# Optimization experiments

Hardware: AMD Instinct MI355X
Metric: run time of the kernel (lower is better)

## Reference

```python
import jax, jax.numpy as jnp
import numpy as np

NOISE = 0.02
P_CONST = 1.0
NUM_LAYERS = 7


def setup_inputs() -> dict:
    key = jax.random.key(0)
    k1, k2, k3, k4 = jax.random.split(key, 4)
    B, Nt, K, L = 2048, 64, 40, NUM_LAYERS
    sqrtP = np.sqrt(P_CONST)
    return {
        'H_real': jax.random.normal(k1, (B, Nt, K), dtype=jnp.float32),
        'H_imag': jax.random.normal(k2, (B, Nt, K), dtype=jnp.float32),
        'eta': jnp.ones((L,), dtype=jnp.float32) * (0.1 / sqrtP),
        'U': jax.random.normal(k3, (L, Nt, Nt), dtype=jnp.float32) * (0.01 / sqrtP),
        'b': jax.random.normal(k4, (L, Nt, K), dtype=jnp.float32) * (0.01 / sqrtP),
    }


def _rate_total(Wr, Wi, Hc):
    # sum over batch of (sum_k log2(1+sinr_k) - power_penalty)
    W = Wr + 1j * Wi                                   # [B,Nt,K] complex
    HW = jnp.einsum('bnk,bnl->bkl', jnp.conj(Hc), W)   # [B,K,K]
    pw = jnp.abs(HW) ** 2                              # |h_k^H w_l|^2
    desired = jnp.diagonal(pw, axis1=1, axis2=2)       # [B,K]
    interference = pw.sum(axis=2) - desired
    sinr = desired / (interference + NOISE)
    rates = jnp.log2(1.0 + sinr).sum()
    power = jnp.sum(Wr * Wr + Wi * Wi, axis=(1, 2))    # ||W||_F^2 per batch
    penalty = jnp.mean((power - P_CONST) ** 2) * 0.01
    B = Wr.shape[0]
    return rates - B * penalty


def reference(H_real, H_imag, eta, U, b):
    Hc = H_real + 1j * H_imag
    B, Nt, K = H_real.shape
    Wr = jnp.zeros((B, Nt, K), dtype=jnp.float32)
    Wi = jnp.zeros((B, Nt, K), dtype=jnp.float32)
    grad_fn = jax.grad(_rate_total, argnums=(0, 1))
    for t in range(NUM_LAYERS):
        g_r, g_i = grad_fn(Wr, Wi, Hc)                 # torch grad: dL/dx + i dL/dy
        Ug_r = jnp.einsum('nm,bmk->bnk', U[t], g_r)
        Ug_i = jnp.einsum('nm,bmk->bnk', U[t], g_i)
        step_r = Ug_r - Ug_i
        step_i = Ug_i + Ug_r
        Wr = Wr - eta[t] * step_r + b[t]
        Wi = Wi - eta[t] * step_i
    # final power normalization
    norm = jnp.sqrt(jnp.sum(Wr * Wr + Wi * Wi, axis=(1, 2), keepdims=True))
    scale = jnp.sqrt(P_CONST) / (norm + 1e-6)
    Wr = Wr * scale
    Wi = Wi * scale
    return Wr + 1j * Wi
```

## Files before the change

kernel.cpp:

```cpp
#include <hip/hip_runtime.h>
#include <math.h>

typedef _Float16 h16;
typedef __attribute__((ext_vector_type(2))) _Float16 h16x2;
typedef __attribute__((ext_vector_type(4))) _Float16 h16x4;
typedef __attribute__((ext_vector_type(8))) _Float16 h16x8;
typedef __attribute__((ext_vector_type(4))) float f32x4;

#define NBATCH 2048
#define NT 64
#define KK 40
#define NL 7
#define SIGMA 0.02f
#define INVLN2 1.4426950408889634f

#define WT   0
#define HCK  (48*128)
#define HNC  (HCK + 48*128)
#define B2T  (HNC + 64*128)
#define GRE  B2T
#define GIM  (B2T + 48*64)
#define UOF  (B2T + 48*128)
#define LDSH (UOF + 64*64)

#define SWZ(row, c)  ((c) ^ (((row)&7)<<3))
#define SWZW(row, c) ((c) ^ (((row)&15)<<3))
#define MFMA16(a,b,c) __builtin_amdgcn_mfma_f32_16x16x32_f16((a),(b),(c),0,0,0)

static __device__ __forceinline__ float DOT2(h16x2 a, h16x2 b, float c) {
#if __has_builtin(__builtin_amdgcn_fdot2)
    return __builtin_amdgcn_fdot2(a, b, c, false);
#else
    return fmaf((float)a.x, (float)b.x, fmaf((float)a.y, (float)b.y, c));
#endif
}
static __device__ __forceinline__ h16x2 PK(float x, float y) {
    h16x2 r; r.x = (h16)x; r.y = (h16)y; return r;
}
static __device__ __forceinline__ h16x8 conjA(h16x8 v) {
    union { h16x8 h; unsigned u[4]; } x; x.h = v;
    #pragma unroll
    for (int i=0;i<4;++i){ unsigned t=x.u[i]; t=(t>>16)|(t<<16); x.u[i]=t^0x80000000u; }
    return x.h;
}
static __device__ __forceinline__ h16x8 imB(h16x8 v) {
    union { h16x8 h; unsigned u[4]; } x; x.h = v;
    #pragma unroll
    for (int i=0;i<4;++i){ unsigned t=x.u[i]; t=(t>>16)|(t<<16); x.u[i]=t^0x00008000u; }
    return x.h;
}

__global__ __launch_bounds__(256, 2) void gpnet_kernel(
    const float* __restrict__ gHr, const float* __restrict__ gHi,
    const float* __restrict__ gEta, const float* __restrict__ gU,
    const float* __restrict__ gB, float* __restrict__ gOut, int outFloats)
{
    __shared__ __align__(16) h16 sh[LDSH];
    __shared__ float sRed[4];

    const int tid = threadIdx.x;
    const int wv  = tid >> 6;
    const int ln  = tid & 63;
    const int col = ln & 15;
    const int g   = ln >> 4;

    const int bb = blockIdx.x;
    const float* hr = gHr + (size_t)bb * NT * KK;
    const float* hi = gHi + (size_t)bb * NT * KK;

    for (int i = tid; i < 512; i += 256) {
        *(h16x2*)(sh + WT  + 40*128 + 2*i) = PK(0.f, 0.f);
        *(h16x2*)(sh + HCK + 40*128 + 2*i) = PK(0.f, 0.f);
    }
    for (int i = tid; i < 512; i += 256) {
        int n = i >> 3, c = 80 + 2*(i & 7);
        *(h16x2*)(sh + HNC + n*128 + SWZ(n, c)) = PK(0.f, 0.f);
    }
    for (int i = tid; i < NT*KK; i += 256) {
        int n = i / KK, k = i % KK;
        float xr = hr[i], xi = hi[i];
        h16x2 p = PK(xr, xi);
        *(h16x2*)(sh + HCK + k*128 + SWZW(k, 2*n)) = p;
        *(h16x2*)(sh + HNC + n*128 + SWZ(n, 2*k)) = p;
        *(h16x2*)(sh + WT  + k*128 + SWZW(k, 2*n)) = PK(gB[i], 0.f);
    }
    float Wr[3][4], Wi[3][4];
    float ps = 0.f;
    #pragma unroll
    for (int ct = 0; ct < 3; ++ct)
        #pragma unroll
        for (int r = 0; r < 4; ++r) {
            int n = 16*wv + 4*g + r, l = col + 16*ct;
            float b0 = (l < KK) ? gB[n*KK + l] : 0.f;
            Wr[ct][r] = b0; Wi[ct][r] = 0.f;
            ps += b0 * b0;
        }
    #pragma unroll
    for (int off = 32; off; off >>= 1) ps += __shfl_down(ps, off, 64);
    if (ln == 0) sRed[wv] = ps;
    __syncthreads();

    for (int t = 1; t < NL; ++t) {
        const float pw   = sRed[0] + sRed[1] + sRed[2] + sRed[3];
        const float cpen = 0.04f * (pw - 1.0f);
        const float etat = gEta[t];

        float2 ureg[8];
        {
            const float2* u2 = (const float2*)(gU + (size_t)t * NT * NT);
            #pragma unroll
            for (int j = 0; j < 8; ++j) ureg[j] = u2[tid + j*256];
        }
        float breg[3][4];
        #pragma unroll
        for (int ct = 0; ct < 3; ++ct)
            #pragma unroll
            for (int r = 0; r < 4; ++r) {
                int n = 16*wv + 4*g + r, l = col + 16*ct;
                breg[ct][r] = (l < KK) ? gB[(size_t)t*NT*KK + n*KK + l] : 0.f;
            }

        if (wv < 3) {
            f32x4 aRe[3], aIm[3];
            #pragma unroll
            for (int rt = 0; rt < 3; ++rt) { aRe[rt] = (f32x4){0.f,0.f,0.f,0.f}; aIm[rt] = (f32x4){0.f,0.f,0.f,0.f}; }
            const int kcol = col + 16*wv;
            #pragma unroll
            for (int q = 0; q < 4; ++q) {
                h16x8 bf = *(const h16x8*)(sh + HCK + kcol*128 + SWZW(kcol, g*8 + 32*q));
                #pragma unroll
                for (int rt = 0; rt < 3; ++rt) {
                    int lrow = col + 16*rt;
                    h16x8 af = *(const h16x8*)(sh + WT + lrow*128 + SWZW(lrow, g*8 + 32*q));
                    aRe[rt] = MFMA16(af, bf, aRe[rt]);
                    aIm[rt] = MFMA16(conjA(af), bf, aIm[rt]);
                }
            }
            #pragma unroll
            for (int rt = 0; rt < 3; ++rt)
                #pragma unroll
                for (int r = 0; r < 4; ++r) {
                    int l = 16*rt + 4*g + r;
                    *(h16x2*)(sh + B2T + l*128 + SWZ(l, 2*kcol)) =
                        PK(aRe[rt][r], aIm[rt][r]);
                }
        }
        __syncthreads();

        if (tid < 160) {
            const int k = tid >> 2, q = tid & 3;
            h16x2 va[10];
            #pragma unroll
            for (int ii = 0; ii < 10; ++ii)
                va[ii] = *(const h16x2*)(sh + B2T + (q*10+ii)*128 + SWZ(q*10+ii, 2*k));
            float rs = 0.f, dd = 0.f;
            #pragma unroll
            for (int ii = 0; ii < 10; ++ii) rs = DOT2(va[ii], va[ii], rs);
            const int dk = k - q*10;
            if (dk >= 0 && dk < 10) dd = DOT2(va[dk], va[dk], 0.f);
            rs += __shfl_xor(rs, 1, 64); rs += __shfl_xor(rs, 2, 64);
            dd += __shfl_xor(dd, 1, 64); dd += __shfl_xor(dd, 2, 64);
            float T  = rs + SIGMA, Is = rs - dd + SIGMA;
            float cA_ = 2.f * INVLN2 / T;
            float cC_ = -2.f * INVLN2 * dd / (Is * T);
            #pragma unroll
            for (int ii = 0; ii < 10; ++ii) {
                int l = q*10 + ii;
                float c = (l == k) ? cA_ : cC_;
                *(h16x2*)(sh + B2T + l*128 + SWZ(l, 2*k)) =
                    PK((float)va[ii].x * c, -(float)va[ii].y * c);
            }
        }
        __syncthreads();

        f32x4 gRe[3], gIm[3];
        #pragma unroll
        for (int ct = 0; ct < 3; ++ct) { gRe[ct] = (f32x4){0.f,0.f,0.f,0.f}; gIm[ct] = (f32x4){0.f,0.f,0.f,0.f}; }
        {
            const int nrow = col + 16*wv;
            #pragma unroll
            for (int q = 0; q < 3; ++q) {
                h16x8 af = *(const h16x8*)(sh + HNC + nrow*128 + SWZ(nrow, g*8 + 32*q));
                #pragma unroll
                for (int ct = 0; ct < 3; ++ct) {
                    int lr = col + 16*ct;
                    h16x8 bf = *(const h16x8*)(sh + B2T + lr*128 + SWZ(lr, g*8 + 32*q));
                    gRe[ct] = MFMA16(af, bf, gRe[ct]);
                    gIm[ct] = MFMA16(af, imB(bf), gIm[ct]);
                }
            }
        }
        #pragma unroll
        for (int j = 0; j < 8; ++j) {
            int e2 = tid + j*256;
            int n = e2 >> 5, m2 = (e2 & 31) * 2;
            *(h16x2*)(sh + UOF + n*64 + SWZ(n, m2)) = PK(ureg[j].x, ureg[j].y);
        }
        __syncthreads();
        {
            const int n0w = 16*wv + 4*g;
            #pragma unroll
            for (int ct = 0; ct < 3; ++ct) {
                int l = col + 16*ct;
                h16x4 g4, q4;
                #pragma unroll
                for (int r = 0; r < 4; ++r) {
                    g4[r] = (h16)(gRe[ct][r] - cpen * Wr[ct][r]);
                    q4[r] = (h16)(gIm[ct][r] - cpen * Wi[ct][r]);
                }
                *(h16x4*)(sh + GRE + l*64 + SWZ(l, n0w)) = g4;
                *(h16x4*)(sh + GIM + l*64 + SWZ(l, n0w)) = q4;
            }
        }
        __syncthreads();

        f32x4 cRe[3], cIm[3];
        #pragma unroll
        for (int ct = 0; ct < 3; ++ct) { cRe[ct] = (f32x4){0.f,0.f,0.f,0.f}; cIm[ct] = (f32x4){0.f,0.f,0.f,0.f}; }
        {
            const int nrow = col + 16*wv;
            #pragma unroll
            for (int q = 0; q < 2; ++q) {
                h16x8 af = *(const h16x8*)(sh + UOF + nrow*64 + SWZ(nrow, g*8 + 32*q));
                #pragma unroll
                for (int ct = 0; ct < 3; ++ct) {
                    const int l = col + 16*ct;
                    h16x8 fre = *(const h16x8*)(sh + GRE + l*64 + SWZ(l, g*8 + 32*q));
                    h16x8 fim = *(const h16x8*)(sh + GIM + l*64 + SWZ(l, g*8 + 32*q));
                    cRe[ct] = MFMA16(af, fre, cRe[ct]);
                    cIm[ct] = MFMA16(af, fim, cIm[ct]);
                }
            }
        }
        float ps2 = 0.f;
        {
            const int n0w = 16*wv + 4*g;
            #pragma unroll
            for (int ct = 0; ct < 3; ++ct) {
                int l = col + 16*ct;
                h16x8 wvv;
                #pragma unroll
                for (int r = 0; r < 4; ++r) {
                    float ur = cRe[ct][r], ui = cIm[ct][r];
                    float wr = Wr[ct][r] - etat*(ur - ui) + breg[ct][r];
                    float wi = Wi[ct][r] - etat*(ui + ur);
                    Wr[ct][r] = wr; Wi[ct][r] = wi;
                    wvv[2*r]   = (h16)wr;
                    wvv[2*r+1] = (h16)wi;
                    if (l < KK) ps2 += wr*wr + wi*wi;
                }
                if (l < KK)
                    *(h16x8*)(sh + WT + l*128 + SWZW(l, 2*n0w)) = wvv;
            }
        }
        #pragma unroll
        for (int off = 32; off; off >>= 1) ps2 += __shfl_down(ps2, off, 64);
        if (ln == 0) sRed[wv] = ps2;
        __syncthreads();
    }

    const float pwf   = sRed[0] + sRed[1] + sRed[2] + sRed[3];
    const float scale = 1.0f / (sqrtf(pwf) + 1e-6f);

    if (outFloats >= 2 * NBATCH * NT * KK) {
        float2* ob = (float2*)(gOut + (size_t)bb * NT * KK * 2);
        #pragma unroll
        for (int ct = 0; ct < 3; ++ct)
            #pragma unroll
            for (int r = 0; r < 4; ++r) {
                int n = 16*wv + 4*g + r, l = col + 16*ct;
                if (l < KK) {
                    float2 v; v.x = Wr[ct][r]*scale; v.y = Wi[ct][r]*scale;
                    ob[n*KK + l] = v;
                }
            }
    } else {
        float* ob = gOut + (size_t)bb * NT * KK;
        #pragma unroll
        for (int ct = 0; ct < 3; ++ct)
            #pragma unroll
            for (int r = 0; r < 4; ++r) {
                int n = 16*wv + 4*g + r, l = col + 16*ct;
                if (l < KK) ob[n*KK + l] = Wr[ct][r] * scale;
            }
    }
}

extern "C" void kernel_launch(void* const* d_in, const int* in_sizes, int n_in,
                              void* d_out, int out_size, void* d_ws, size_t ws_size,
                              hipStream_t stream) {
    (void)in_sizes; (void)n_in; (void)d_ws; (void)ws_size;
    const float* Hr  = (const float*)d_in[0];
    const float* Hi  = (const float*)d_in[1];
    const float* eta = (const float*)d_in[2];
    const float* U   = (const float*)d_in[3];
    const float* b   = (const float*)d_in[4];
    float* out = (float*)d_out;
    gpnet_kernel<<<NBATCH, 256, 0, stream>>>(Hr, Hi, eta, U, b, out, out_size);
}
```

Baseline: 116.9 us.

## Ping-pong W/B2 LDS buffers and load U in idle wave to drop a barrier

Replaces the fixed W buffer and B2/G scratch with two alternating LDS regions, so the updated W can be written into the region freed after the gradient stage. The idle fourth wave loads the U matrix into LDS during the first MFMA stage instead of every thread staging it through registers. This removes one __syncthreads per layer and the register pressure from holding U. In exchange the padding rows of the alternating buffer are re-zeroed each layer and one wave does all the U global loads.

```diff
diff --git a/kernel.cpp b/kernel.cpp
--- a/kernel.cpp
+++ b/kernel.cpp
@@ -14,13 +14,11 @@
 #define SIGMA 0.02f
 #define INVLN2 1.4426950408889634f
 
-#define WT   0
-#define HCK  (48*128)
+#define RA   0
+#define RB   (48*128)
+#define HCK  (2*48*128)
 #define HNC  (HCK + 48*128)
-#define B2T  (HNC + 64*128)
-#define GRE  B2T
-#define GIM  (B2T + 48*64)
-#define UOF  (B2T + 48*128)
+#define UOF  (HNC + 64*128)
 #define LDSH (UOF + 64*64)
 
 #define SWZ(row, c)  ((c) ^ (((row)&7)<<3))
@@ -69,7 +67,7 @@
     const float* hi = gHi + (size_t)bb * NT * KK;
 
     for (int i = tid; i < 512; i += 256) {
-        *(h16x2*)(sh + WT  + 40*128 + 2*i) = PK(0.f, 0.f);
+        *(h16x2*)(sh + RA  + 40*128 + 2*i) = PK(0.f, 0.f);
         *(h16x2*)(sh + HCK + 40*128 + 2*i) = PK(0.f, 0.f);
     }
     for (int i = tid; i < 512; i += 256) {
@@ -82,7 +80,7 @@
         h16x2 p = PK(xr, xi);
         *(h16x2*)(sh + HCK + k*128 + SWZW(k, 2*n)) = p;
         *(h16x2*)(sh + HNC + n*128 + SWZ(n, 2*k)) = p;
-        *(h16x2*)(sh + WT  + k*128 + SWZW(k, 2*n)) = PK(gB[i], 0.f);
+        *(h16x2*)(sh + RA  + k*128 + SWZW(k, 2*n)) = PK(gB[i], 0.f);
     }
     float Wr[3][4], Wi[3][4];
     float ps = 0.f;
@@ -101,16 +99,14 @@
     __syncthreads();
 
     for (int t = 1; t < NL; ++t) {
+        const int P = (t & 1) ? RA : RB;
+        const int Q = (t & 1) ? RB : RA;
+        const int GREo = P, GIMo = P + 48*64;
+
         const float pw   = sRed[0] + sRed[1] + sRed[2] + sRed[3];
         const float cpen = 0.04f * (pw - 1.0f);
         const float etat = gEta[t];
 
-        float2 ureg[8];
-        {
-            const float2* u2 = (const float2*)(gU + (size_t)t * NT * NT);
-            #pragma unroll
-            for (int j = 0; j < 8; ++j) ureg[j] = u2[tid + j*256];
-        }
         float breg[3][4];
         #pragma unroll
         for (int ct = 0; ct < 3; ++ct)
@@ -131,7 +127,7 @@
                 #pragma unroll
                 for (int rt = 0; rt < 3; ++rt) {
                     int lrow = col + 16*rt;
-                    h16x8 af = *(const h16x8*)(sh + WT + lrow*128 + SWZW(lrow, g*8 + 32*q));
+                    h16x8 af = *(const h16x8*)(sh + P + lrow*128 + SWZW(lrow, g*8 + 32*q));
                     aRe[rt] = MFMA16(af, bf, aRe[rt]);
                     aIm[rt] = MFMA16(conjA(af), bf, aIm[rt]);
                 }
@@ -141,9 +137,18 @@
                 #pragma unroll
                 for (int r = 0; r < 4; ++r) {
                     int l = 16*rt + 4*g + r;
-                    *(h16x2*)(sh + B2T + l*128 + SWZ(l, 2*kcol)) =
+                    *(h16x2*)(sh + Q + l*128 + SWZ(l, 2*kcol)) =
                         PK(aRe[rt][r], aIm[rt][r]);
                 }
+        } else {
+            const float2* u2 = (const float2*)(gU + (size_t)t * NT * NT);
+            #pragma unroll 8
+            for (int j = 0; j < 32; ++j) {
+                int e2 = j*64 + ln;
+                float2 v = u2[e2];
+                int n = e2 >> 5, m2 = (e2 & 31) * 2;
+                *(h16x2*)(sh + UOF + n*64 + SWZ(n, m2)) = PK(v.x, v.y);
+            }
         }
         __syncthreads();
 
@@ -152,7 +157,7 @@
             h16x2 va[10];
             #pragma unroll
             for (int ii = 0; ii < 10; ++ii)
-                va[ii] = *(const h16x2*)(sh + B2T + (q*10+ii)*128 + SWZ(q*10+ii, 2*k));
+                va[ii] = *(const h16x2*)(sh + Q + (q*10+ii)*128 + SWZ(q*10+ii, 2*k));
             float rs = 0.f, dd = 0.f;
             #pragma unroll
             for (int ii = 0; ii < 10; ++ii) rs = DOT2(va[ii], va[ii], rs);
@@ -167,7 +172,7 @@
             for (int ii = 0; ii < 10; ++ii) {
                 int l = q*10 + ii;
                 float c = (l == k) ? cA_ : cC_;
-                *(h16x2*)(sh + B2T + l*128 + SWZ(l, 2*k)) =
+                *(h16x2*)(sh + Q + l*128 + SWZ(l, 2*k)) =
                     PK((float)va[ii].x * c, -(float)va[ii].y * c);
             }
         }
@@ -184,19 +189,12 @@
                 #pragma unroll
                 for (int ct = 0; ct < 3; ++ct) {
                     int lr = col + 16*ct;
-                    h16x8 bf = *(const h16x8*)(sh + B2T + lr*128 + SWZ(lr, g*8 + 32*q));
+                    h16x8 bf = *(const h16x8*)(sh + Q + lr*128 + SWZ(lr, g*8 + 32*q));
                     gRe[ct] = MFMA16(af, bf, gRe[ct]);
                     gIm[ct] = MFMA16(af, imB(bf), gIm[ct]);
                 }
             }
         }
-        #pragma unroll
-        for (int j = 0; j < 8; ++j) {
-            int e2 = tid + j*256;
-            int n = e2 >> 5, m2 = (e2 & 31) * 2;
-            *(h16x2*)(sh + UOF + n*64 + SWZ(n, m2)) = PK(ureg[j].x, ureg[j].y);
-        }
-        __syncthreads();
         {
             const int n0w = 16*wv + 4*g;
             #pragma unroll
@@ -208,8 +206,8 @@
                     g4[r] = (h16)(gRe[ct][r] - cpen * Wr[ct][r]);
                     q4[r] = (h16)(gIm[ct][r] - cpen * Wi[ct][r]);
                 }
-                *(h16x4*)(sh + GRE + l*64 + SWZ(l, n0w)) = g4;
-                *(h16x4*)(sh + GIM + l*64 + SWZ(l, n0w)) = q4;
+                *(h16x4*)(sh + GREo + l*64 + SWZ(l, n0w)) = g4;
+                *(h16x4*)(sh + GIMo + l*64 + SWZ(l, n0w)) = q4;
             }
         }
         __syncthreads();
@@ -225,8 +223,8 @@
                 #pragma unroll
                 for (int ct = 0; ct < 3; ++ct) {
                     const int l = col + 16*ct;
-                    h16x8 fre = *(const h16x8*)(sh + GRE + l*64 + SWZ(l, g*8 + 32*q));
-                    h16x8 fim = *(const h16x8*)(sh + GIM + l*64 + SWZ(l, g*8 + 32*q));
+                    h16x8 fre = *(const h16x8*)(sh + GREo + l*64 + SWZ(l, g*8 + 32*q));
+                    h16x8 fim = *(const h16x8*)(sh + GIMo + l*64 + SWZ(l, g*8 + 32*q));
                     cRe[ct] = MFMA16(af, fre, cRe[ct]);
                     cIm[ct] = MFMA16(af, fim, cIm[ct]);
                 }
@@ -250,8 +248,10 @@
                     if (l < KK) ps2 += wr*wr + wi*wi;
                 }
                 if (l < KK)
-                    *(h16x8*)(sh + WT + l*128 + SWZW(l, 2*n0w)) = wvv;
-            }
+                    *(h16x8*)(sh + Q + l*128 + SWZW(l, 2*n0w)) = wvv;
+            }
+            h16x4 z4; z4[0] = (h16)0.f; z4[1] = (h16)0.f; z4[2] = (h16)0.f; z4[3] = (h16)0.f;
+            *(h16x4*)(sh + Q + 40*128 + 4*tid) = z4;
         }
         #pragma unroll
         for (int off = 32; off; off >>= 1) ps2 += __shfl_down(ps2, off, 64);
```

New measurement: 114.2 us. 1.02x faster.
